# Kernel optimization log

Hardware: AMD Instinct MI355X
Metric: run time of the kernel (lower is better)

The kernel has to match this reference:

```python
import jax, jax.numpy as jnp
import numpy as np


def setup_inputs() -> dict:
    key = jax.random.key(0)
    ks = jax.random.split(key, 6)
    B, S, H = 1, 512, 2048
    NH, D = 16, 128
    S_CACHE = 8192
    TOPK = 16
    hidden_states = jax.random.normal(ks[0], (B, S, H), dtype=jnp.float32)
    Wqkv = jax.random.normal(ks[1], (3 * H, H), dtype=jnp.float32) * 0.02
    Wout = jax.random.normal(ks[2], (H, H), dtype=jnp.float32) * 0.02
    k_cache = jax.random.normal(ks[3], (B, NH, S_CACHE, D), dtype=jnp.float32)
    v_cache = jax.random.normal(ks[4], (B, NH, S_CACHE, D), dtype=jnp.float32)
    position_bias = jax.random.normal(ks[5], (NH, S, S), dtype=jnp.float32) * 0.1
    # causal mask: True = masked out (matches torch masked_fill semantics)
    attention_mask = ~jnp.tril(jnp.ones((S, S), dtype=bool))
    return {
        "hidden_states": hidden_states,
        "Wqkv": Wqkv,
        "Wout": Wout,
        "k_cache": k_cache,
        "v_cache": v_cache,
        "position_bias": position_bias,
        "attention_mask": attention_mask,
        "topk": TOPK,
    }


SIM_THRESHOLD = 0.25  # config.sim_threshold


def reference(hidden_states, Wqkv, Wout, k_cache, v_cache, position_bias,
              attention_mask, topk):
    B, S, H = hidden_states.shape
    NH, D = k_cache.shape[1], k_cache.shape[3]
    scale = 1.0 / jnp.sqrt(jnp.asarray(D, hidden_states.dtype))

    # QKV projection (Linear, no bias): x @ W^T, then split heads
    qkv = jnp.einsum('bsh,oh->bso', hidden_states, Wqkv)
    q, k, v = jnp.split(qkv, 3, axis=-1)
    def to_heads(x):
        return x.reshape(B, S, NH, D).transpose(0, 2, 1, 3)  # [B,NH,S,D]
    q, k, v = to_heads(q), to_heads(k), to_heads(v)

    # local attention scores + alibi-style bias
    scores_local = jnp.einsum('bhqd,bhkd->bhqk', q, k) * scale
    scores_local = scores_local + position_bias[None]  # [B,NH,S,S]

    # cosine-similarity retrieval over long-range cache
    q_n = q / jnp.linalg.norm(q, axis=-1, keepdims=True)
    k_n = k_cache / jnp.linalg.norm(k_cache, axis=-1, keepdims=True)
    sim = jnp.einsum('bhqd,bhkd->bhqk', q_n, k_n)  # [B,NH,S,S_CACHE]
    val, idx = jax.lax.top_k(sim, topk)            # [B,NH,S,topk]
    reshaped_idx = idx.reshape(B, NH, S * topk)

    # gather retrieved K/V
    sel_k = jnp.take_along_axis(k_cache, reshaped_idx[..., None], axis=2)  # [B,NH,S*topk,D]
    sel_v = jnp.take_along_axis(v_cache, reshaped_idx[..., None], axis=2)

    scores_cache = jnp.einsum('bhqd,bhkd->bhqk', q, sel_k) * scale  # [B,NH,S,S*topk]
    neg = jnp.finfo(scores_cache.dtype).min

    # similarity-threshold mask (mask_by_sim=True)
    sim_mask = ~(val > SIM_THRESHOLD)                       # [B,NH,S,topk]
    sim_mask = sim_mask.reshape(B, NH, 1, S * topk)         # broadcast over queries
    scores_cache = jnp.where(sim_mask, neg, scores_cache)

    # block-diagonal external-memory mask: query i attends only to its own topk slots
    rows = jnp.arange(S)[:, None]
    cols_block = jnp.arange(S * topk)[None, :] // topk
    ext_mask = cols_block != rows                           # [S, S*topk], True = masked

    full_mask = jnp.concatenate([ext_mask, attention_mask], axis=1)  # [S, S*topk+S]
    scores = jnp.concatenate([scores_cache, scores_local], axis=-1)
    scores = jnp.where(full_mask[None, None], neg, scores)

    attn = jax.nn.softmax(scores.astype(jnp.float32), axis=-1).astype(v.dtype)
    values = jnp.concatenate([sel_v, v], axis=2)            # [B,NH,S*topk+S,D]
    ctx = jnp.einsum('bhqk,bhkd->bhqd', attn, values)
    ctx = ctx.transpose(0, 2, 1, 3).reshape(B, S, H)
    attn_output = jnp.einsum('bsh,oh->bso', ctx, Wout)
    return attn_output
```

## Files before the change

kernel.cpp:

```cpp
#include <hip/hip_runtime.h>

typedef _Float16 half8 __attribute__((ext_vector_type(8)));
typedef _Float16 half4 __attribute__((ext_vector_type(4)));
typedef _Float16 half2t __attribute__((ext_vector_type(2)));
typedef float f32x4 __attribute__((ext_vector_type(4)));
typedef float f32x2 __attribute__((ext_vector_type(2)));

#define NHEAD 16
#define SEQ 512
#define DIM 128
#define HID 2048
#define SCACHE 8192
#define CAP 64
#define SCALE 0.08838834764831845f
#define NEG_INF (-__builtin_inff())

__global__ __launch_bounds__(256) void gemm_xwT(const float* __restrict__ A,
                                                const float* __restrict__ B,
                                                float* __restrict__ Cpart,
                                                int K, int gridN, int kslices) {
  __shared__ __align__(16) _Float16 As[128][84];
  __shared__ __align__(16) _Float16 Bs[128][84];
  int b = blockIdx.x;
  int kblk = b % kslices;
  int nm = b / kslices;
  int nblk = nm % gridN, mblk = nm / gridN;
  int N = gridN * 128;
  int kchunk = K / kslices;
  int t = threadIdx.x;
  int lane = t & 63, wid = t >> 6;
  int wm = (wid >> 1) * 64, wn = (wid & 1) * 64;
  f32x4 acc[4][4] = {};
  const float* Ab = A + (size_t)mblk * 128 * K;
  const float* Bb = B + (size_t)nblk * 128 * K;
  int rowS = t >> 4, c4 = (t & 15) * 4;

  for (int k0 = kblk * kchunk; k0 < kblk * kchunk + kchunk; k0 += 64) {
#pragma unroll
    for (int i = 0; i < 8; ++i) {
      int row = rowS + 16 * i;
      float4 av = *(const float4*)(Ab + (size_t)row * K + k0 + c4);
      float4 bv = *(const float4*)(Bb + (size_t)row * K + k0 + c4);
      half4 ah = {(_Float16)av.x, (_Float16)av.y, (_Float16)av.z, (_Float16)av.w};
      half4 bh = {(_Float16)bv.x, (_Float16)bv.y, (_Float16)bv.z, (_Float16)bv.w};
      *(half4*)&As[row][c4] = ah;
      *(half4*)&Bs[row][c4] = bh;
    }
    __syncthreads();
#pragma unroll
    for (int ks = 0; ks < 2; ++ks) {
      int ko = ks * 32 + (lane >> 4) * 8;
      int rr = lane & 15;
      half8 af[4], bf[4];
#pragma unroll
      for (int i = 0; i < 4; ++i) af[i] = *(const half8*)&As[wm + i * 16 + rr][ko];
#pragma unroll
      for (int j = 0; j < 4; ++j) bf[j] = *(const half8*)&Bs[wn + j * 16 + rr][ko];
#pragma unroll
      for (int i = 0; i < 4; ++i)
#pragma unroll
        for (int j = 0; j < 4; ++j)
          acc[i][j] = __builtin_amdgcn_mfma_f32_16x16x32_f16(af[i], bf[j], acc[i][j], 0, 0, 0);
    }
    __syncthreads();
  }
  float* Cp = Cpart + (size_t)kblk * ((size_t)gridN * 128) * 512;
  int cR = (lane >> 4) * 4, cC = lane & 15;
#pragma unroll
  for (int i = 0; i < 4; ++i)
#pragma unroll
    for (int j = 0; j < 4; ++j) {
      int row = mblk * 128 + wm + i * 16 + cR;
      int col = nblk * 128 + wn + j * 16 + cC;
#pragma unroll
      for (int r = 0; r < 4; ++r)
        Cp[(size_t)(row + r) * N + col] = acc[i][j][r];
    }
}

__global__ __launch_bounds__(256) void reduce_k(const float* __restrict__ part,
                                                float* __restrict__ dst,
                                                int kslices, int ncol, int dstride) {
  size_t e = ((size_t)blockIdx.x * 256 + threadIdx.x) * 4;
  size_t slice = (size_t)512 * ncol;
  f32x4 s = *(const f32x4*)(part + e);
  for (int p = 1; p < kslices; ++p)
    s += *(const f32x4*)(part + (size_t)p * slice + e);
  size_t row = e / ncol;
  int col = (int)(e % ncol);
  *(f32x4*)(dst + row * dstride + col) = s;
}

__global__ __launch_bounds__(256) void gemm_q_hi(const float* __restrict__ A,
                                                 const float* __restrict__ B,
                                                 float* __restrict__ C) {
  __shared__ __align__(16) _Float16 Ah[64][40], Al[64][40];
  __shared__ __align__(16) _Float16 Bh[64][40], Bl[64][40];
  int b = blockIdx.x;
  int nblk = b & 31, mblk = b >> 5;
  int t = threadIdx.x, lane = t & 63, wid = t >> 6;
  int wm = (wid >> 1) * 32, wn = (wid & 1) * 32;
  int quad = lane >> 4, rr = lane & 15;
  f32x4 acc[2][2] = {};
  const float* Ab = A + (size_t)mblk * 64 * 2048;
  const float* Bb = B + (size_t)nblk * 64 * 2048;
  int rowS = t >> 2, cS = (t & 3) * 8;

  for (int k0 = 0; k0 < 2048; k0 += 32) {
#pragma unroll
    for (int half = 0; half < 2; ++half) {
      int c = cS + half * 4;
      float4 av = *(const float4*)(Ab + (size_t)rowS * 2048 + k0 + c);
      float4 bv = *(const float4*)(Bb + (size_t)rowS * 2048 + k0 + c);
      half4 ah = {(_Float16)av.x, (_Float16)av.y, (_Float16)av.z, (_Float16)av.w};
      half4 bh = {(_Float16)bv.x, (_Float16)bv.y, (_Float16)bv.z, (_Float16)bv.w};
      half4 al = {(_Float16)(av.x - (float)ah.x), (_Float16)(av.y - (float)ah.y),
                  (_Float16)(av.z - (float)ah.z), (_Float16)(av.w - (float)ah.w)};
      half4 bl = {(_Float16)(bv.x - (float)bh.x), (_Float16)(bv.y - (float)bh.y),
                  (_Float16)(bv.z - (float)bh.z), (_Float16)(bv.w - (float)bh.w)};
      *(half4*)&Ah[rowS][c] = ah;
      *(half4*)&Al[rowS][c] = al;
      *(half4*)&Bh[rowS][c] = bh;
      *(half4*)&Bl[rowS][c] = bl;
    }
    __syncthreads();
    int ko = quad * 8;
    half8 afh[2], afl[2], bfh[2], bfl[2];
#pragma unroll
    for (int i = 0; i < 2; ++i) {
      afh[i] = *(const half8*)&Ah[wm + i * 16 + rr][ko];
      afl[i] = *(const half8*)&Al[wm + i * 16 + rr][ko];
      bfh[i] = *(const half8*)&Bh[wn + i * 16 + rr][ko];
      bfl[i] = *(const half8*)&Bl[wn + i * 16 + rr][ko];
    }
#pragma unroll
    for (int i = 0; i < 2; ++i)
#pragma unroll
      for (int j = 0; j < 2; ++j) {
        acc[i][j] = __builtin_amdgcn_mfma_f32_16x16x32_f16(afl[i], bfh[j], acc[i][j], 0, 0, 0);
        acc[i][j] = __builtin_amdgcn_mfma_f32_16x16x32_f16(afh[i], bfl[j], acc[i][j], 0, 0, 0);
        acc[i][j] = __builtin_amdgcn_mfma_f32_16x16x32_f16(afh[i], bfh[j], acc[i][j], 0, 0, 0);
      }
    __syncthreads();
  }
  int cR = quad * 4;
#pragma unroll
  for (int i = 0; i < 2; ++i)
#pragma unroll
    for (int j = 0; j < 2; ++j) {
      int row = mblk * 64 + wm + i * 16 + cR;
      int col = nblk * 64 + wn + j * 16 + rr;
#pragma unroll
      for (int r = 0; r < 4; ++r)
        C[(size_t)(row + r) * (3 * HID) + col] = acc[i][j][r];
    }
}

__global__ __launch_bounds__(256) void cache_norm(const float* __restrict__ kc,
                                                  _Float16* __restrict__ kn16,
                                                  double* __restrict__ kninv) {
  int w = threadIdx.x >> 6, lane = threadIdx.x & 63;
  int row = blockIdx.x * 4 + w;
  f32x2 v = *(const f32x2*)(kc + (size_t)row * DIM + lane * 2);
  double s = (double)v[0] * v[0] + (double)v[1] * v[1];
#pragma unroll
  for (int off = 32; off; off >>= 1) s += __shfl_xor(s, off);
  float inv = rsqrtf((float)s);
  half2t o = {(_Float16)(v[0] * inv), (_Float16)(v[1] * inv)};
  *(half2t*)(kn16 + (size_t)row * DIM + lane * 2) = o;
  if (lane == 0) kninv[row] = 1.0 / sqrt(s);
}

__global__ __launch_bounds__(256) void prep_local(const float* __restrict__ qkv,
                                                  _Float16* __restrict__ q16,
                                                  _Float16* __restrict__ k16,
                                                  _Float16* __restrict__ qn16) {
  int w = threadIdx.x >> 6, lane = threadIdx.x & 63;
  int rid = blockIdx.x * 4 + w;
  int h = rid >> 9, s = rid & 511;
  const float* qp = qkv + (size_t)s * (3 * HID) + h * DIM + lane * 2;
  f32x2 q = *(const f32x2*)qp;
  f32x2 k = *(const f32x2*)(qp + HID);
  float ss = q[0] * q[0] + q[1] * q[1];
#pragma unroll
  for (int off = 32; off; off >>= 1) ss += __shfl_xor(ss, off);
  float inv = rsqrtf(ss);
  half2t qh = {(_Float16)q[0], (_Float16)q[1]};
  half2t kh = {(_Float16)k[0], (_Float16)k[1]};
  half2t qnh = {(_Float16)(q[0] * inv), (_Float16)(q[1] * inv)};
  *(half2t*)(q16 + (size_t)rid * DIM + lane * 2) = qh;
  *(half2t*)(k16 + (size_t)rid * DIM + lane * 2) = kh;
  *(half2t*)(qn16 + (size_t)rid * DIM + lane * 2) = qnh;
}

__global__ __launch_bounds__(256) void sim_cand(const _Float16* __restrict__ qn16,
                                                const _Float16* __restrict__ kn16,
                                                int* __restrict__ cnt,
                                                int* __restrict__ cidx) {
  __shared__ __align__(16) _Float16 Qs[64][132];
  int b = blockIdx.x;
  int h = b & 15, cblk = b >> 4;
  int t = threadIdx.x, lane = t & 63, w = t >> 6;
  int quad = lane >> 4, rr = lane & 15;

  half8 bf[2][4];
  {
    const _Float16* kb = kn16 + ((size_t)(h * SCACHE + cblk * 128 + w * 32)) * DIM;
#pragma unroll
    for (int jn = 0; jn < 2; ++jn)
#pragma unroll
      for (int ks = 0; ks < 4; ++ks)
        bf[jn][ks] = *(const half8*)(kb + (size_t)(jn * 16 + rr) * DIM + ks * 32 + quad * 8);
  }

  for (int qt = 0; qt < 8; ++qt) {
    __syncthreads();
    const _Float16* qb = qn16 + ((size_t)(h * SEQ + qt * 64)) * DIM;
#pragma unroll
    for (int i = 0; i < 4; ++i) {
      int f = t + 256 * i;
      int row = f >> 4, c8 = (f & 15) * 8;
      *(uint4*)&Qs[row][c8] = *(const uint4*)(qb + (size_t)row * DIM + c8);
    }
    __syncthreads();

    f32x4 acc[4][2] = {};
#pragma unroll
    for (int ks = 0; ks < 4; ++ks) {
      int ko = ks * 32 + quad * 8;
      half8 af[4];
#pragma unroll
      for (int i = 0; i < 4; ++i) af[i] = *(const half8*)&Qs[i * 16 + rr][ko];
#pragma unroll
      for (int i = 0; i < 4; ++i)
#pragma unroll
        for (int j = 0; j < 2; ++j)
          acc[i][j] = __builtin_amdgcn_mfma_f32_16x16x32_f16(af[i], bf[j][ks], acc[i][j], 0, 0, 0);
    }
    int qrow_base = qt * 64 + (quad << 2);
    int key_base = cblk * 128 + w * 32 + rr;
#pragma unroll
    for (int i = 0; i < 4; ++i)
#pragma unroll
      for (int j = 0; j < 2; ++j)
#pragma unroll
        for (int r = 0; r < 4; ++r) {
          float v = acc[i][j][r];
          if (v > 0.249f) {
            int q = qrow_base + i * 16 + r;
            int rowid = h * SEQ + q;
            int pos = atomicAdd(&cnt[rowid], 1);
            if (pos < CAP) cidx[rowid * CAP + pos] = key_base + j * 16;
          }
        }
  }
}

__global__ __launch_bounds__(256) void select_topk(const int* __restrict__ cnt,
                                                   const int* __restrict__ cidx,
                                                   const float* __restrict__ qkv,
                                                   const float* __restrict__ kcache,
                                                   const double* __restrict__ kninv,
                                                   int* __restrict__ sel_idx,
                                                   float* __restrict__ sel_score) {
  int w = threadIdx.x >> 6, lane = threadIdx.x & 63;
  int rowid = blockIdx.x * 4 + w;
  int h = rowid >> 9, s = rowid & 511;
  const float* qp = qkv + (size_t)s * (3 * HID) + h * DIM;

  f32x2 qv2 = *(const f32x2*)(qp + lane * 2);
  double qs = (double)qv2[0] * qv2[0] + (double)qv2[1] * qv2[1];
#pragma unroll
  for (int off = 32; off; off >>= 1) qs += __shfl_xor(qs, off);
  double thr = 0.25 * sqrt(qs);

  int n = min(cnt[rowid], CAP);
  int idx = 0x7fffffff;
  double r = -1e300, d = 0.0;
  if (lane < n) {
    idx = cidx[rowid * CAP + lane];
    const float* kp = kcache + ((size_t)(h * SCACHE + idx)) * DIM;
    double d0 = 0.0, d1 = 0.0;
#pragma unroll
    for (int j = 0; j < DIM; j += 8) {
      f32x4 ka = *(const f32x4*)(kp + j);
      f32x4 kb = *(const f32x4*)(kp + j + 4);
      f32x4 qa = *(const f32x4*)(qp + j);
      f32x4 qb = *(const f32x4*)(qp + j + 4);
      d0 = fma((double)qa[0], (double)ka[0], d0);
      d1 = fma((double)qa[1], (double)ka[1], d1);
      d0 = fma((double)qa[2], (double)ka[2], d0);
      d1 = fma((double)qa[3], (double)ka[3], d1);
      d0 = fma((double)qb[0], (double)kb[0], d0);
      d1 = fma((double)qb[1], (double)kb[1], d1);
      d0 = fma((double)qb[2], (double)kb[2], d0);
      d1 = fma((double)qb[3], (double)kb[3], d1);
    }
    d = d0 + d1;
    r = d * kninv[h * SCACHE + idx];
  }

  int rank = 0;
  for (int j = 0; j < n; ++j) {
    double rj = __shfl(r, j);
    int ij = __shfl(idx, j);
    if (rj > r || (rj == r && ij < idx)) ++rank;
  }
  bool sel = (lane < n) && (rank < 16) && (r > thr);
  unsigned long long m = __ballot(sel);
  int nsel = __popcll(m);
  if (sel) {
    int pos = __popcll(m & ((1ull << lane) - 1));
    sel_idx[rowid * 16 + pos] = idx;
    sel_score[rowid * 16 + pos] = (float)(d * (double)SCALE);
  }
  if (lane >= nsel && lane < 16) {
    sel_idx[rowid * 16 + lane] = 0;
    sel_score[rowid * 16 + lane] = NEG_INF;
  }
}

__global__ __launch_bounds__(256) void attn_part(const float* __restrict__ qkv,
                                                 const _Float16* __restrict__ q16,
                                                 const _Float16* __restrict__ k16,
                                                 const float* __restrict__ bias,
                                                 float* __restrict__ part_m,
                                                 float* __restrict__ part_l,
                                                 float* __restrict__ part_o) {
  __shared__ __align__(16) _Float16 Vs[128][136];
  __shared__ __align__(16) _Float16 Ps[16][136];
  __shared__ float mred[16][4], lred[16][4];

  int pb = blockIdx.x;
  int tt = pb % 80, h = pb / 80;
  int qb, cb;
  if (tt < 8)       { qb = tt;                cb = 0; }
  else if (tt < 24) { int u = tt - 8;  qb = 8 + (u >> 1); cb = u & 1; }
  else if (tt < 48) { int u = tt - 24; int q3 = u / 3; qb = 16 + q3; cb = u - q3 * 3; }
  else              { int u = tt - 48; qb = 24 + (u >> 2); cb = u & 3; }
  int q0 = qb * 16, kc0 = cb * 128;

  int t = threadIdx.x, lane = t & 63, w = t >> 6;
  int quad = lane >> 4, col = lane & 15;

  const float* vbase = qkv + 2 * HID + h * DIM;
#pragma unroll
  for (int i = 0; i < 16; ++i) {
    int idx = t + 256 * i;
    int key = idx & 127, dg = idx >> 7;
    f32x4 vv = *(const f32x4*)(vbase + (size_t)(kc0 + key) * (3 * HID) + dg * 4);
#pragma unroll
    for (int e = 0; e < 4; ++e) Vs[dg * 4 + e][key] = (_Float16)vv[e];
  }

  const _Float16* qbp = q16 + ((size_t)(h * SEQ + q0)) * DIM;
  half8 af[4];
#pragma unroll
  for (int ks = 0; ks < 4; ++ks)
    af[ks] = *(const half8*)(qbp + (size_t)col * DIM + ks * 32 + quad * 8);

  f32x4 acc[2] = {};
#pragma unroll
  for (int jn = 0; jn < 2; ++jn) {
    const _Float16* kp = k16 + ((size_t)(h * SEQ + kc0 + w * 32 + jn * 16 + col)) * DIM;
#pragma unroll
    for (int ks = 0; ks < 4; ++ks) {
      half8 bf = *(const half8*)(kp + ks * 32 + quad * 8);
      acc[jn] = __builtin_amdgcn_mfma_f32_16x16x32_f16(af[ks], bf, acc[jn], 0, 0, 0);
    }
  }
  float s[2][4];
#pragma unroll
  for (int jn = 0; jn < 2; ++jn) {
    int keyg = kc0 + w * 32 + jn * 16 + col;
#pragma unroll
    for (int r = 0; r < 4; ++r) {
      int qrow = q0 + quad * 4 + r;
      float sv = NEG_INF;
      if (keyg <= qrow)
        sv = acc[jn][r] * SCALE + bias[((size_t)h * SEQ + qrow) * SEQ + keyg];
      s[jn][r] = sv;
    }
  }

  float mw[4];
#pragma unroll
  for (int r = 0; r < 4; ++r) {
    float m = fmaxf(s[0][r], s[1][r]);
#pragma unroll
    for (int off = 1; off < 16; off <<= 1) m = fmaxf(m, __shfl_xor(m, off));
    mw[r] = m;
  }
  if (col == 0)
#pragma unroll
    for (int r = 0; r < 4; ++r) mred[quad * 4 + r][w] = mw[r];
  __syncthreads();

  float M[4];
#pragma unroll
  for (int r = 0; r < 4; ++r) {
    int row = quad * 4 + r;
    float m = fmaxf(fmaxf(mred[row][0], mred[row][1]),
                    fmaxf(mred[row][2], mred[row][3]));
    M[r] = m;
    float p0 = __expf(s[0][r] - m);
    float p1 = __expf(s[1][r] - m);
    Ps[row][w * 32 + col] = (_Float16)p0;
    Ps[row][w * 32 + 16 + col] = (_Float16)p1;
    float l = p0 + p1;
#pragma unroll
    for (int off = 1; off < 16; off <<= 1) l += __shfl_xor(l, off);
    if (col == 0) lred[row][w] = l;
  }
  if (w == 0 && col == 0)
#pragma unroll
    for (int r = 0; r < 4; ++r) part_m[pb * 16 + quad * 4 + r] = M[r];
  __syncthreads();

  f32x4 o[2] = {};
#pragma unroll
  for (int jn = 0; jn < 2; ++jn) {
#pragma unroll
    for (int ks = 0; ks < 4; ++ks) {
      half8 a = *(const half8*)&Ps[col][ks * 32 + quad * 8];
      half8 bv = *(const half8*)&Vs[w * 32 + jn * 16 + col][ks * 32 + quad * 8];
      o[jn] = __builtin_amdgcn_mfma_f32_16x16x32_f16(a, bv, o[jn], 0, 0, 0);
    }
  }
#pragma unroll
  for (int jn = 0; jn < 2; ++jn)
#pragma unroll
    for (int r = 0; r < 4; ++r)
      part_o[((size_t)pb * 16 + quad * 4 + r) * 128 + w * 32 + jn * 16 + col] = o[jn][r];
  if (t < 16)
    part_l[pb * 16 + t] = lred[t][0] + lred[t][1] + lred[t][2] + lred[t][3];
}

__global__ __launch_bounds__(256) void attn_merge(const float* __restrict__ part_m,
                                                  const float* __restrict__ part_l,
                                                  const float* __restrict__ part_o,
                                                  const int* __restrict__ sel_idx,
                                                  const float* __restrict__ sel_score,
                                                  const float* __restrict__ vcache,
                                                  float* __restrict__ ctx) {
  int w = threadIdx.x >> 6, lane = threadIdx.x & 63;
  int row = blockIdx.x * 4 + w;
  int h = row >> 9, q = row & 511;
  int qb = q >> 4, r = q & 15;
  int base = (qb < 8) ? qb
           : (qb < 16) ? 8 + 2 * (qb - 8)
           : (qb < 24) ? 24 + 3 * (qb - 16)
                       : 48 + 4 * (qb - 24);
  int ncb = (qb >> 3) + 1;
  int pb0 = h * 80 + base;

  float scv[16], mc = NEG_INF;
#pragma unroll
  for (int j = 0; j < 16; ++j) {
    scv[j] = sel_score[row * 16 + j];
    mc = fmaxf(mc, scv[j]);
  }
  float mi[4];
  float M = mc;
  for (int i = 0; i < ncb; ++i) {
    mi[i] = part_m[(pb0 + i) * 16 + r];
    M = fmaxf(M, mi[i]);
  }
  f32x2 O = {0.f, 0.f};
  float L = 0.f;
  for (int i = 0; i < ncb; ++i) {
    float sc = __expf(mi[i] - M);
    f32x2 ov = *(const f32x2*)(part_o + ((size_t)(pb0 + i) * 16 + r) * 128 + lane * 2);
    O += ov * sc;
    L += part_l[(pb0 + i) * 16 + r] * sc;
  }
#pragma unroll
  for (int j = 0; j < 16; ++j) {
    if (scv[j] > NEG_INF) {
      float wv = __expf(scv[j] - M);
      int idx = sel_idx[row * 16 + j];
      f32x2 v = *(const f32x2*)(vcache + ((size_t)(h * SCACHE + idx)) * DIM + lane * 2);
      O += v * wv;
      L += wv;
    }
  }
  f32x2 res = O * (1.f / L);
  *(f32x2*)(ctx + (size_t)q * HID + h * DIM + lane * 2) = res;
}

extern "C" void kernel_launch(void* const* d_in, const int* in_sizes, int n_in,
                              void* d_out, int out_size, void* d_ws, size_t ws_size,
                              hipStream_t stream) {
  const float* hidden = (const float*)d_in[0];
  const float* Wqkv   = (const float*)d_in[1];
  const float* Wout   = (const float*)d_in[2];
  const float* kcache = (const float*)d_in[3];
  const float* vcache = (const float*)d_in[4];
  const float* bias   = (const float*)d_in[5];

  char* ws = (char*)d_ws;
  size_t off = 0;
  float*    qkv   = (float*)(ws + off);    off += (size_t)SEQ * 3 * HID * 4;
  _Float16* q16   = (_Float16*)(ws + off); off += (size_t)NHEAD * SEQ * DIM * 2;
  _Float16* k16   = (_Float16*)(ws + off); off += (size_t)NHEAD * SEQ * DIM * 2;
  _Float16* qn16  = (_Float16*)(ws + off); off += (size_t)NHEAD * SEQ * DIM * 2;
  _Float16* kn16  = (_Float16*)(ws + off); off += (size_t)NHEAD * SCACHE * DIM * 2;
  double*   kninv = (double*)(ws + off);   off += (size_t)NHEAD * SCACHE * 8;
  int*      ccnt  = (int*)(ws + off);      off += (size_t)NHEAD * SEQ * 4;
  int*      cidx  = (int*)(ws + off);      off += (size_t)NHEAD * SEQ * CAP * 4;
  int*      selidx  = (int*)(ws + off);    off += (size_t)NHEAD * SEQ * 16 * 4;
  float*    selsc   = (float*)(ws + off);  off += (size_t)NHEAD * SEQ * 16 * 4;
  float*    ctx   = (float*)(ws + off);    off += (size_t)SEQ * HID * 4;
  float*    pm    = (float*)(ws + off);    off += (size_t)1280 * 16 * 4;
  float*    pl    = (float*)(ws + off);    off += (size_t)1280 * 16 * 4;
  float*    po    = (float*)(ws + off);    off += (size_t)1280 * 16 * 128 * 4;
  float*    gpart = (float*)(ws + off);

  hipMemsetAsync(ccnt, 0, (size_t)NHEAD * SEQ * 4, stream);
  cache_norm<<<dim3(NHEAD * SCACHE / 4), dim3(256), 0, stream>>>(kcache, kn16, kninv);
  gemm_xwT<<<dim3(4 * 32 * 4), dim3(256), 0, stream>>>(hidden, Wqkv + (size_t)2048 * 2048,
                                                       gpart, 2048, 32, 4);
  reduce_k<<<dim3(SEQ * 4096 / 1024), dim3(256), 0, stream>>>(gpart, qkv + 2048, 4, 4096,
                                                              3 * HID);
  gemm_q_hi<<<dim3(256), dim3(256), 0, stream>>>(hidden, Wqkv, qkv);
  prep_local<<<dim3(NHEAD * SEQ / 4), dim3(256), 0, stream>>>(qkv, q16, k16, qn16);
  sim_cand<<<dim3(NHEAD * 64), dim3(256), 0, stream>>>(qn16, kn16, ccnt, cidx);
  select_topk<<<dim3(NHEAD * SEQ / 4), dim3(256), 0, stream>>>(ccnt, cidx, qkv, kcache,
                                                               kninv, selidx, selsc);
  attn_part<<<dim3(16 * 80), dim3(256), 0, stream>>>(qkv, q16, k16, bias, pm, pl, po);
  attn_merge<<<dim3(NHEAD * SEQ / 4), dim3(256), 0, stream>>>(pm, pl, po, selidx, selsc,
                                                              vcache, ctx);
  gemm_xwT<<<dim3(4 * 16 * 8), dim3(256), 0, stream>>>(ctx, Wout, gpart, 2048, 16, 8);
  reduce_k<<<dim3(SEQ * 2048 / 1024), dim3(256), 0, stream>>>(gpart, (float*)d_out, 8, 2048,
                                                              2048);
}
```

Before: 495.8 us.

## Pre-split Q projection operands into fp16 hi/lo and use smaller GEMM tiles

The fp32-to-fp16 hi/lo split for the hidden states and the Q rows of Wqkv moves out of the GEMM inner loop into a separate elementwise kernel, which writes fp16 buffers into the gpart scratch area. The Q GEMM then loads pre-split fp16 tiles with 32x32 output blocks and 1024 blocks instead of 64x64 and 256, to raise occupancy and parallelism. In exchange it adds two kernel launches and extra global memory traffic for the split buffers, and each loaded tile is reused less. Reusing gpart is safe because reduce_k has already consumed it.

```diff
diff --git a/kernel.cpp b/kernel.cpp
--- a/kernel.cpp
+++ b/kernel.cpp
@@ -91,69 +91,62 @@
   *(f32x4*)(dst + row * dstride + col) = s;
 }
 
-__global__ __launch_bounds__(256) void gemm_q_hi(const float* __restrict__ A,
-                                                 const float* __restrict__ B,
+__global__ __launch_bounds__(256) void split_hilo(const float* __restrict__ src,
+                                                  _Float16* __restrict__ hi,
+                                                  _Float16* __restrict__ lo) {
+  size_t e = ((size_t)blockIdx.x * 256 + threadIdx.x) * 4;
+  f32x4 v = *(const f32x4*)(src + e);
+  half4 h = {(_Float16)v[0], (_Float16)v[1], (_Float16)v[2], (_Float16)v[3]};
+  half4 l = {(_Float16)(v[0] - (float)h[0]), (_Float16)(v[1] - (float)h[1]),
+             (_Float16)(v[2] - (float)h[2]), (_Float16)(v[3] - (float)h[3])};
+  *(half4*)(hi + e) = h;
+  *(half4*)(lo + e) = l;
+}
+
+__global__ __launch_bounds__(256) void gemm_q_hi(const _Float16* __restrict__ Ahg,
+                                                 const _Float16* __restrict__ Alg,
+                                                 const _Float16* __restrict__ Bhg,
+                                                 const _Float16* __restrict__ Blg,
                                                  float* __restrict__ C) {
-  __shared__ __align__(16) _Float16 Ah[64][40], Al[64][40];
-  __shared__ __align__(16) _Float16 Bh[64][40], Bl[64][40];
+  __shared__ __align__(16) _Float16 Ahs[32][72], Als[32][72];
+  __shared__ __align__(16) _Float16 Bhs[32][72], Bls[32][72];
   int b = blockIdx.x;
-  int nblk = b & 31, mblk = b >> 5;
-  int t = threadIdx.x, lane = t & 63, wid = t >> 6;
-  int wm = (wid >> 1) * 32, wn = (wid & 1) * 32;
+  int nblk = b & 63, mblk = b >> 6;
+  int t = threadIdx.x, lane = t & 63, w = t >> 6;
+  int wm = (w >> 1) * 16, wn = (w & 1) * 16;
   int quad = lane >> 4, rr = lane & 15;
-  f32x4 acc[2][2] = {};
-  const float* Ab = A + (size_t)mblk * 64 * 2048;
-  const float* Bb = B + (size_t)nblk * 64 * 2048;
-  int rowS = t >> 2, cS = (t & 3) * 8;
-
-  for (int k0 = 0; k0 < 2048; k0 += 32) {
-#pragma unroll
-    for (int half = 0; half < 2; ++half) {
-      int c = cS + half * 4;
-      float4 av = *(const float4*)(Ab + (size_t)rowS * 2048 + k0 + c);
-      float4 bv = *(const float4*)(Bb + (size_t)rowS * 2048 + k0 + c);
-      half4 ah = {(_Float16)av.x, (_Float16)av.y, (_Float16)av.z, (_Float16)av.w};
-      half4 bh = {(_Float16)bv.x, (_Float16)bv.y, (_Float16)bv.z, (_Float16)bv.w};
-      half4 al = {(_Float16)(av.x - (float)ah.x), (_Float16)(av.y - (float)ah.y),
-                  (_Float16)(av.z - (float)ah.z), (_Float16)(av.w - (float)ah.w)};
-      half4 bl = {(_Float16)(bv.x - (float)bh.x), (_Float16)(bv.y - (float)bh.y),
-                  (_Float16)(bv.z - (float)bh.z), (_Float16)(bv.w - (float)bh.w)};
-      *(half4*)&Ah[rowS][c] = ah;
-      *(half4*)&Al[rowS][c] = al;
-      *(half4*)&Bh[rowS][c] = bh;
-      *(half4*)&Bl[rowS][c] = bl;
-    }
+  f32x4 acc = {};
+  const _Float16* Ab0 = Ahg + (size_t)(mblk * 32) * 2048;
+  const _Float16* Ab1 = Alg + (size_t)(mblk * 32) * 2048;
+  const _Float16* Bb0 = Bhg + (size_t)(nblk * 32) * 2048;
+  const _Float16* Bb1 = Blg + (size_t)(nblk * 32) * 2048;
+  int srow = t >> 3, sc = (t & 7) * 8;
+
+  for (int k0 = 0; k0 < 2048; k0 += 64) {
+    size_t goff = (size_t)srow * 2048 + k0 + sc;
+    *(uint4*)&Ahs[srow][sc] = *(const uint4*)(Ab0 + goff);
+    *(uint4*)&Als[srow][sc] = *(const uint4*)(Ab1 + goff);
+    *(uint4*)&Bhs[srow][sc] = *(const uint4*)(Bb0 + goff);
+    *(uint4*)&Bls[srow][sc] = *(const uint4*)(Bb1 + goff);
     __syncthreads();
-    int ko = quad * 8;
-    half8 afh[2], afl[2], bfh[2], bfl[2];
-#pragma unroll
-    for (int i = 0; i < 2; ++i) {
-      afh[i] = *(const half8*)&Ah[wm + i * 16 + rr][ko];
-      afl[i] = *(const half8*)&Al[wm + i * 16 + rr][ko];
-      bfh[i] = *(const half8*)&Bh[wn + i * 16 + rr][ko];
-      bfl[i] = *(const half8*)&Bl[wn + i * 16 + rr][ko];
-    }
-#pragma unroll
-    for (int i = 0; i < 2; ++i)
-#pragma unroll
-      for (int j = 0; j < 2; ++j) {
-        acc[i][j] = __builtin_amdgcn_mfma_f32_16x16x32_f16(afl[i], bfh[j], acc[i][j], 0, 0, 0);
-        acc[i][j] = __builtin_amdgcn_mfma_f32_16x16x32_f16(afh[i], bfl[j], acc[i][j], 0, 0, 0);
-        acc[i][j] = __builtin_amdgcn_mfma_f32_16x16x32_f16(afh[i], bfh[j], acc[i][j], 0, 0, 0);
-      }
+#pragma unroll
+    for (int ks = 0; ks < 2; ++ks) {
+      int ko = ks * 32 + quad * 8;
+      half8 afh = *(const half8*)&Ahs[wm + rr][ko];
+      half8 afl = *(const half8*)&Als[wm + rr][ko];
+      half8 bfh = *(const half8*)&Bhs[wn + rr][ko];
+      half8 bfl = *(const half8*)&Bls[wn + rr][ko];
+      acc = __builtin_amdgcn_mfma_f32_16x16x32_f16(afl, bfh, acc, 0, 0, 0);
+      acc = __builtin_amdgcn_mfma_f32_16x16x32_f16(afh, bfl, acc, 0, 0, 0);
+      acc = __builtin_amdgcn_mfma_f32_16x16x32_f16(afh, bfh, acc, 0, 0, 0);
+    }
     __syncthreads();
   }
-  int cR = quad * 4;
-#pragma unroll
-  for (int i = 0; i < 2; ++i)
-#pragma unroll
-    for (int j = 0; j < 2; ++j) {
-      int row = mblk * 64 + wm + i * 16 + cR;
-      int col = nblk * 64 + wn + j * 16 + rr;
-#pragma unroll
-      for (int r = 0; r < 4; ++r)
-        C[(size_t)(row + r) * (3 * HID) + col] = acc[i][j][r];
-    }
+  int row = mblk * 32 + wm + quad * 4;
+  int col = nblk * 32 + wn + rr;
+#pragma unroll
+  for (int r = 0; r < 4; ++r)
+    C[(size_t)(row + r) * (3 * HID) + col] = acc[r];
 }
 
 __global__ __launch_bounds__(256) void cache_norm(const float* __restrict__ kc,
@@ -515,6 +508,10 @@
   float*    pl    = (float*)(ws + off);    off += (size_t)1280 * 16 * 4;
   float*    po    = (float*)(ws + off);    off += (size_t)1280 * 16 * 128 * 4;
   float*    gpart = (float*)(ws + off);
+  _Float16* Ahg = (_Float16*)gpart;
+  _Float16* Alg = Ahg + (size_t)SEQ * HID;
+  _Float16* Bhg = Alg + (size_t)SEQ * HID;
+  _Float16* Blg = Bhg + (size_t)HID * HID;
 
   hipMemsetAsync(ccnt, 0, (size_t)NHEAD * SEQ * 4, stream);
   cache_norm<<<dim3(NHEAD * SCACHE / 4), dim3(256), 0, stream>>>(kcache, kn16, kninv);
@@ -522,7 +519,9 @@
                                                        gpart, 2048, 32, 4);
   reduce_k<<<dim3(SEQ * 4096 / 1024), dim3(256), 0, stream>>>(gpart, qkv + 2048, 4, 4096,
                                                               3 * HID);
-  gemm_q_hi<<<dim3(256), dim3(256), 0, stream>>>(hidden, Wqkv, qkv);
+  split_hilo<<<dim3(SEQ * HID / 1024), dim3(256), 0, stream>>>(hidden, Ahg, Alg);
+  split_hilo<<<dim3(HID * HID / 1024), dim3(256), 0, stream>>>(Wqkv, Bhg, Blg);
+  gemm_q_hi<<<dim3(1024), dim3(256), 0, stream>>>(Ahg, Alg, Bhg, Blg, qkv);
   prep_local<<<dim3(NHEAD * SEQ / 4), dim3(256), 0, stream>>>(qkv, q16, k16, qn16);
   sim_cand<<<dim3(NHEAD * 64), dim3(256), 0, stream>>>(qn16, kn16, ccnt, cidx);
   select_topk<<<dim3(NHEAD * SEQ / 4), dim3(256), 0, stream>>>(ccnt, cidx, qkv, kcache,
```

Result: faster. 456.3 us (-8.0%).
